# Kernel optimization log

Hardware: AMD Instinct MI355X
Metric: run time of the kernel (lower is better)

Reference implementation:

```python
import jax, jax.numpy as jnp
import numpy as np

B, S, DIN, DIM, H = 2, 2304, 1024, 1024, 16
HEAD_DIM = DIM // H            # 64
ROT_DIM = HEAD_DIM             # partial_rotary_factor = 1
BASE = 10000.0
EPS = 1e-6


def setup_inputs() -> dict:
    key = jax.random.key(0)
    ks = jax.random.split(key, 6)
    return {
        "input": jax.random.normal(ks[0], (B, S, DIN), dtype=jnp.float32),
        "qkv_w": jax.random.normal(ks[1], (3 * DIM, DIN), dtype=jnp.float32) * 0.02,
        "qkv_b": jnp.zeros((3 * DIM,), dtype=jnp.float32),
        "q_scale": jnp.ones((DIM,), dtype=jnp.float32),
        "k_scale": jnp.ones((DIM,), dtype=jnp.float32),
        "proj_w": jax.random.normal(ks[2], (DIN, DIM), dtype=jnp.float32) * 0.02,
        "proj_b": jnp.zeros((DIN,), dtype=jnp.float32),
        "height": 48,
        "width": 48,
    }


def _rms_norm(x, scale):
    # RMSNorm over the full inner dim (QKNorm), learned scale
    var = jnp.mean(x * x, axis=-1, keepdims=True)
    return x * jax.lax.rsqrt(var + EPS) * scale


def _rope_1d(x, pos):
    # x: (b, n, h, d_ax), pos: (n,) float; rotate_half-style RoPE
    d = x.shape[-1]
    inv_freq = 1.0 / (BASE ** (jnp.arange(0, d, 2, dtype=jnp.float32) / d))  # (d/2,)
    ang = pos[:, None] * inv_freq                                            # (n, d/2)
    cos = jnp.concatenate([jnp.cos(ang), jnp.cos(ang)], axis=-1)[None, :, None, :]
    sin = jnp.concatenate([jnp.sin(ang), jnp.sin(ang)], axis=-1)[None, :, None, :]
    x1, x2 = jnp.split(x, 2, axis=-1)
    rot = jnp.concatenate([-x2, x1], axis=-1)
    return x * cos + rot * sin


def _rope_2d(x, height, width):
    # axial 2D RoPE: first half of rotary dims keyed by row, second half by col
    n = height * width
    idx = jnp.arange(n, dtype=jnp.float32)
    rows = jnp.floor(idx / width)
    cols = jnp.mod(idx, width)
    half = ROT_DIM // 2
    x_r = _rope_1d(x[..., :half], rows)
    x_c = _rope_1d(x[..., half:ROT_DIM], cols)
    return jnp.concatenate([x_r, x_c, x[..., ROT_DIM:]], axis=-1)


def reference(input, qkv_w, qkv_b, q_scale, k_scale, proj_w, proj_b, height, width):
    b, n, _ = input.shape
    qkv = input @ qkv_w.T + qkv_b                       # (b, n, 3*dim)
    q, k, v = jnp.split(qkv, 3, axis=-1)
    q = _rms_norm(q, q_scale)
    k = _rms_norm(k, k_scale)
    # (b, n, h, d)
    q = q.reshape(b, n, H, HEAD_DIM)
    k = k.reshape(b, n, H, HEAD_DIM)
    v = v.reshape(b, n, H, HEAD_DIM)
    q = _rope_2d(q, height, width)
    k = _rope_2d(k, height, width)
    scale = HEAD_DIM ** (-0.5)
    # (b, h, q, k)
    scores = jnp.einsum("bqhd,bkhd->bhqk", q, k) * scale
    attn = jax.nn.softmax(scores, axis=-1)
    out = jnp.einsum("bhqk,bkhd->bqhd", attn, v)        # (b, n, h, d)
    out = out.reshape(b, n, DIM)
    return out @ proj_w.T + proj_b
```

## Files before the change

kernel.cpp:

```cpp
#include <hip/hip_runtime.h>
#include <math.h>

#define BB   2
#define SS   2304
#define DINC 1024
#define DIMC 1024
#define HH   16
#define HD   64

typedef _Float16 half_t;
typedef __attribute__((ext_vector_type(4))) _Float16 half4;
typedef __attribute__((ext_vector_type(8))) _Float16 half8;
typedef __attribute__((ext_vector_type(4))) float    f32x4;

#define LOG2E 1.44269504088896340736f
#define EXP2(x) __builtin_amdgcn_exp2f(x)

#define GLOAD_LDS16(gp, lp)                                                     \
    __builtin_amdgcn_global_load_lds(                                           \
        (const __attribute__((address_space(1))) void*)(gp),                    \
        (__attribute__((address_space(3))) void*)(lp), 16, 0, 0)

template<int RB>
__global__ __launch_bounds__(256)
void convert_tile_f16(const float* __restrict__ src, half_t* __restrict__ dst, int K)
{
    constexpr int NG = RB * 32 / 1024;
    const int mb = blockIdx.x;
    const int kb = blockIdx.y;
    const int t  = threadIdx.x;
    const float* sp0 = src + (size_t)mb * RB * K + kb * 32;
    half_t*      dp0 = dst + ((size_t)mb * (K >> 5) + kb) * (RB * 32);
    #pragma unroll
    for (int g = 0; g < NG; ++g) {
        const int e  = g * 1024 + t * 4;
        const int mm = e >> 5, kk = e & 31;
        float4 v = *(const float4*)(sp0 + (size_t)mm * K + kk);
        dp0[e + 0] = (half_t)v.x; dp0[e + 1] = (half_t)v.y;
        dp0[e + 2] = (half_t)v.z; dp0[e + 3] = (half_t)v.w;
    }
}

__global__ __launch_bounds__(256, 3)
void gemm_mfma192(const half_t* __restrict__ Ah, const half_t* __restrict__ Bh,
                  const float* __restrict__ bias, half_t* __restrict__ Cout)
{
    const int t    = threadIdx.x;
    const int w    = t >> 6;
    const int lane = t & 63;
    const int l15  = lane & 15, quad = lane >> 4;
    const int wr   = w >> 1;
    const int wc   = w & 1;
    const int mb   = blockIdx.y;
    const int nb   = blockIdx.x;

    __shared__ __align__(16) half_t As[2][6144];
    __shared__ __align__(16) half_t Bs[2][3072];

    f32x4 acc[6][3];
    #pragma unroll
    for (int mt = 0; mt < 6; ++mt)
        #pragma unroll
        for (int nt = 0; nt < 3; ++nt) acc[mt][nt] = (f32x4){0.f, 0.f, 0.f, 0.f};

    const half_t* atile = Ah + (size_t)mb * 32 * 6144;
    const half_t* btile = Bh + (size_t)nb * 32 * 3072;

    for (int kb = 0; kb < 32; kb += 2) {
        #pragma unroll
        for (int u = 0; u < 2; ++u) {
            const half_t* at = atile + (size_t)(kb + u) * 6144;
            const half_t* bt = btile + (size_t)(kb + u) * 3072;
            for (int ch = w; ch < 18; ch += 4) {
                if (ch < 12) GLOAD_LDS16(at + ch * 512 + lane * 8, &As[u][ch * 512]);
                else         GLOAD_LDS16(bt + (ch - 12) * 512 + lane * 8,
                                         &Bs[u][(ch - 12) * 512]);
            }
        }
        __syncthreads();

        #pragma unroll
        for (int u = 0; u < 2; ++u) {
            half8 af[6], bf[3];
            #pragma unroll
            for (int mt = 0; mt < 6; ++mt)
                af[mt] = *(const half8*)(&As[u][(wr * 96 + mt * 16 + l15) * 32 + quad * 8]);
            #pragma unroll
            for (int nt = 0; nt < 3; ++nt)
                bf[nt] = *(const half8*)(&Bs[u][(wc * 48 + nt * 16 + l15) * 32 + quad * 8]);
            #pragma unroll
            for (int mt = 0; mt < 6; ++mt)
                #pragma unroll
                for (int nt = 0; nt < 3; ++nt)
                    acc[mt][nt] = __builtin_amdgcn_mfma_f32_16x16x32_f16(
                        af[mt], bf[nt], acc[mt][nt], 0, 0, 0);
        }
        __syncthreads();
    }

    const int bm = mb * 192, bn = nb * 96;
    #pragma unroll
    for (int nt = 0; nt < 3; ++nt) {
        const int n  = bn + wc * 48 + nt * 16 + l15;
        const float bv = bias[n];
        #pragma unroll
        for (int mt = 0; mt < 6; ++mt) {
            const int m0 = bm + wr * 96 + mt * 16 + quad * 4;
            #pragma unroll
            for (int rg = 0; rg < 4; ++rg)
                Cout[(size_t)(m0 + rg) * 3072 + n] = (half_t)(acc[mt][nt][rg] + bv);
        }
    }
}

template<int BN, bool OUT_HALF>
__global__ __launch_bounds__(256)
void gemm_mfma(const half_t* __restrict__ Ah, const half_t* __restrict__ Bh,
               const float* __restrict__ bias, void* __restrict__ Cout,
               int M, int N, int K)
{
    constexpr int MT = (BN == 128) ? 4 : 2;
    constexpr int NT = 4;
    const int KB = K >> 5;
    __shared__ half_t As[8192];
    __shared__ half_t Bs[2 * BN * 32];

    const int t    = threadIdx.x;
    const int w    = t >> 6;
    const int lane = t & 63;
    const int l15  = lane & 15, quad = lane >> 4;
    const int wr   = (BN == 128) ? (w >> 1) : w;
    const int wc   = (BN == 128) ? (w & 1) : 0;
    const int mb   = blockIdx.y, nb = blockIdx.x;

    f32x4 acc[MT][NT];
    #pragma unroll
    for (int mt = 0; mt < MT; ++mt)
        #pragma unroll
        for (int nt = 0; nt < NT; ++nt) acc[mt][nt] = (f32x4){0.f, 0.f, 0.f, 0.f};

    const half_t* atile = Ah + (size_t)mb * KB * 4096;
    const half_t* btile = Bh + (size_t)nb * KB * (BN * 32);

    for (int kb = 0; kb < KB; kb += 2) {
        #pragma unroll
        for (int u = 0; u < 2; ++u) {
            const half_t* at = atile + (size_t)(kb + u) * 4096;
            const half_t* bt = btile + (size_t)(kb + u) * (BN * 32);
            #pragma unroll
            for (int v = 0; v < 2; ++v) {
                const int ch = w * 2 + v;
                GLOAD_LDS16(at + ch * 512 + lane * 8, As + u * 4096 + ch * 512);
            }
            GLOAD_LDS16(bt + w * 512 + lane * 8, Bs + u * (BN * 32) + w * 512);
        }
        __syncthreads();

        #pragma unroll
        for (int u = 0; u < 2; ++u) {
            half8 af[MT], bf[NT];
            #pragma unroll
            for (int mt = 0; mt < MT; ++mt)
                af[mt] = *(const half8*)(As + u * 4096
                                         + (wr * (MT * 16) + mt * 16 + l15) * 32 + quad * 8);
            #pragma unroll
            for (int nt = 0; nt < NT; ++nt)
                bf[nt] = *(const half8*)(Bs + u * (BN * 32)
                                         + (wc * 64 + nt * 16 + l15) * 32 + quad * 8);
            #pragma unroll
            for (int mt = 0; mt < MT; ++mt)
                #pragma unroll
                for (int nt = 0; nt < NT; ++nt)
                    acc[mt][nt] = __builtin_amdgcn_mfma_f32_16x16x32_f16(
                        af[mt], bf[nt], acc[mt][nt], 0, 0, 0);
        }
        __syncthreads();
    }

    const int bm = mb * 128, bn = nb * BN;
    #pragma unroll
    for (int nt = 0; nt < NT; ++nt) {
        const int n  = bn + wc * 64 + nt * 16 + l15;
        const float bv = bias[n];
        #pragma unroll
        for (int mt = 0; mt < MT; ++mt) {
            const int m0 = bm + wr * (MT * 16) + mt * 16 + quad * 4;
            #pragma unroll
            for (int rg = 0; rg < 4; ++rg) {
                const float v = acc[mt][nt][rg] + bv;
                if (OUT_HALF) ((half_t*)Cout)[(size_t)(m0 + rg) * N + n] = (half_t)v;
                else          ((float*) Cout)[(size_t)(m0 + rg) * N + n] = v;
            }
        }
    }
}

__global__ __launch_bounds__(256)
void normrope_v7(half_t* __restrict__ qkvh, const float* __restrict__ q_scale,
                 const float* __restrict__ k_scale, const int* __restrict__ wptr,
                 half_t* __restrict__ Kf, half_t* __restrict__ Vf)
{
    const int token = blockIdx.x;
    const int s     = token % SS;
    const int b     = token / SS;
    const int w     = *wptr;
    const int t     = threadIdx.x;
    const float rowp = (float)(s / w);
    const float colp = (float)(s % w);

    half_t* base = qkvh + (size_t)token * 3072;

    const int c    = s >> 5;
    const int slot = s & 31;
    const int ktile = (slot >> 2) & 1;
    const int krow  = ((slot >> 3) << 2) + (slot & 3);

    {
        half4 v4 = *(const half4*)(base + 2048 + 4 * t);
        const int dabs0 = 4 * t;
        const int h  = dabs0 >> 6;
        const int sl3 = slot >> 3, sl7 = slot & 7;
        half_t* vdst = Vf + ((size_t)(b * HH + h) * 72 + c) * 2048;
        #pragma unroll
        for (int ii = 0; ii < 4; ++ii) {
            const int d = (dabs0 + ii) & 63;
            vdst[(d >> 4) * 512 + (sl3 * 16 + (d & 15)) * 8 + sl7] = v4[ii];
        }
    }

    __shared__ float buf[DIMC];
    __shared__ float red[4];

    #pragma unroll
    for (int sel = 0; sel < 2; ++sel) {
        half_t* row = base + sel * DIMC;
        const float* scp = sel ? k_scale : q_scale;

        half4 xh = *(const half4*)(row + 4 * t);
        float x0 = (float)xh[0], x1 = (float)xh[1], x2 = (float)xh[2], x3 = (float)xh[3];
        float ss = x0 * x0 + x1 * x1 + x2 * x2 + x3 * x3;
        #pragma unroll
        for (int o = 32; o >= 1; o >>= 1) ss += __shfl_xor(ss, o);
        if ((t & 63) == 0) red[t >> 6] = ss;
        __syncthreads();

        const float rinv = rsqrtf((red[0] + red[1] + red[2] + red[3]) * (1.0f / DIMC) + 1e-6f);
        float4 g = *(const float4*)(scp + 4 * t);
        buf[4 * t + 0] = x0 * rinv * g.x;
        buf[4 * t + 1] = x1 * rinv * g.y;
        buf[4 * t + 2] = x2 * rinv * g.z;
        buf[4 * t + 3] = x3 * rinv * g.w;
        __syncthreads();

        const float qsc = sel ? 1.0f : (0.125f * LOG2E);

        #pragma unroll
        for (int pp = 0; pp < 2; ++pp) {
            const int p = t + pp * 256;
            const int h = p >> 5;
            const int r = p & 31;
            const int j = r & 15;
            const float pos = (r < 16) ? rowp : colp;
            const int d1 = (r < 16) ? j : (32 + j);
            const int d2 = d1 + 16;
            const float freq = exp2f((float)j * -0.83048202372f);
            const float ang  = pos * freq;
            float sn, cs;
            __sincosf(ang, &sn, &cs);
            const float a1 = buf[h * HD + d1], a2 = buf[h * HD + d2];
            const float o1 = (a1 * cs - a2 * sn) * qsc;
            const float o2 = (a2 * cs + a1 * sn) * qsc;
            if (sel == 0) {
                row[h * HD + d1] = (half_t)o1;
                row[h * HD + d2] = (half_t)o2;
            } else {
                half_t* kdst = Kf + ((size_t)(b * HH + h) * 72 + c) * 2048;
                kdst[((ktile << 1) + (d1 >> 5)) * 512
                     + ((((d1 & 31) >> 3) << 4) + krow) * 8 + (d1 & 7)] = (half_t)o1;
                kdst[((ktile << 1) + (d2 >> 5)) * 512
                     + ((((d2 & 31) >> 3) << 4) + krow) * 8 + (d2 & 7)] = (half_t)o2;
            }
        }
        __syncthreads();
    }
}

__global__ __launch_bounds__(256, 3)
void flash_attn_mfma17(const half_t* __restrict__ qkvh, const half_t* __restrict__ Kf,
                       const half_t* __restrict__ Vf, half_t* __restrict__ attn_h)
{
    const int flat = blockIdx.x;
    const int xcd  = flat & 7;
    const int idx  = flat >> 3;
    const int bh   = xcd * 4 + idx / 24;
    const int qtb  = idx % 24;
    const int b    = bh >> 4, h = bh & 15;
    const int t    = threadIdx.x;
    const int w    = t >> 6;
    const int qh   = w >> 1;
    const int jt   = w & 1;
    const int lane = t & 63;
    const int l15  = lane & 15, quad = lane >> 4;

    const size_t tb = (size_t)b * SS;
    const int q0 = qtb * 96;

    __shared__ float mlb[4][48];
    __shared__ float Ob[2][64][49];

    half8 qf[3][2];
    #pragma unroll
    for (int qt = 0; qt < 3; ++qt)
        #pragma unroll
        for (int dg = 0; dg < 2; ++dg)
            qf[qt][dg] = *(const half8*)(qkvh + (tb + q0 + qh * 48 + qt * 16 + l15) * 3072
                                          + h * HD + dg * 32 + quad * 8);

    const half8 onesA = (l15 == 0)
        ? (half8){(half_t)1, (half_t)1, (half_t)1, (half_t)1,
                  (half_t)1, (half_t)1, (half_t)1, (half_t)1}
        : (half8){(half_t)0, (half_t)0, (half_t)0, (half_t)0,
                  (half_t)0, (half_t)0, (half_t)0, (half_t)0};

    f32x4 acc[4][3];
    f32x4 acc5[3];
    #pragma unroll
    for (int qt = 0; qt < 3; ++qt) {
        acc5[qt] = (f32x4){0.f, 0.f, 0.f, 0.f};
        #pragma unroll
        for (int dt = 0; dt < 4; ++dt) acc[dt][qt] = (f32x4){0.f, 0.f, 0.f, 0.f};
    }

    const half_t* kpl = Kf + (size_t)bh * 147456 + jt * 2048 + lane * 8;
    const half_t* vpl = Vf + (size_t)bh * 147456 + jt * 2048 + lane * 8;

    half8 k00 = *(const half8*)(kpl);
    half8 k01 = *(const half8*)(kpl + 512);
    half8 k10 = *(const half8*)(kpl + 1024);
    half8 k11 = *(const half8*)(kpl + 1536);
    half8 v0  = *(const half8*)(vpl);
    half8 v1  = *(const half8*)(vpl + 512);
    half8 v2  = *(const half8*)(vpl + 1024);
    half8 v3  = *(const half8*)(vpl + 1536);

    const f32x4 initC = (f32x4){-4.f, -4.f, -4.f, -4.f};

    for (int p = 0; p < 36; ++p) {
        f32x4 scA[3], scB[3];
        __builtin_amdgcn_s_setprio(1);
        #pragma unroll
        for (int qt = 0; qt < 3; ++qt) {
            scA[qt] = initC;
            scA[qt] = __builtin_amdgcn_mfma_f32_16x16x32_f16(k00, qf[qt][0], scA[qt], 0, 0, 0);
            scA[qt] = __builtin_amdgcn_mfma_f32_16x16x32_f16(k01, qf[qt][1], scA[qt], 0, 0, 0);
            scB[qt] = initC;
            scB[qt] = __builtin_amdgcn_mfma_f32_16x16x32_f16(k10, qf[qt][0], scB[qt], 0, 0, 0);
            scB[qt] = __builtin_amdgcn_mfma_f32_16x16x32_f16(k11, qf[qt][1], scB[qt], 0, 0, 0);
        }
        __builtin_amdgcn_s_setprio(0);

        if (p + 1 < 36) {
            const half_t* kN = kpl + (size_t)(p + 1) * 4096;
            k00 = *(const half8*)(kN);
            k01 = *(const half8*)(kN + 512);
            k10 = *(const half8*)(kN + 1024);
            k11 = *(const half8*)(kN + 1536);
        }

        half8 pf[3];
        #pragma unroll
        for (int qt = 0; qt < 3; ++qt) {
            const float a0 = EXP2(scA[qt][0]);
            const float a1 = EXP2(scA[qt][1]);
            const float a2 = EXP2(scA[qt][2]);
            const float a3 = EXP2(scA[qt][3]);
            const float b0 = EXP2(scB[qt][0]);
            const float b1 = EXP2(scB[qt][1]);
            const float b2 = EXP2(scB[qt][2]);
            const float b3 = EXP2(scB[qt][3]);
            pf[qt] = (half8){(half_t)a0, (half_t)a1, (half_t)a2, (half_t)a3,
                             (half_t)b0, (half_t)b1, (half_t)b2, (half_t)b3};
        }

        __builtin_amdgcn_s_setprio(1);
        #pragma unroll
        for (int dt = 0; dt < 4; ++dt) {
            const half8 vf = (dt == 0) ? v0 : (dt == 1) ? v1 : (dt == 2) ? v2 : v3;
            #pragma unroll
            for (int qt = 0; qt < 3; ++qt)
                acc[dt][qt] = __builtin_amdgcn_mfma_f32_16x16x32_f16(
                    vf, pf[qt], acc[dt][qt], 0, 0, 0);
        }
        #pragma unroll
        for (int qt = 0; qt < 3; ++qt)
            acc5[qt] = __builtin_amdgcn_mfma_f32_16x16x32_f16(
                onesA, pf[qt], acc5[qt], 0, 0, 0);
        __builtin_amdgcn_s_setprio(0);

        if (p + 1 < 36) {
            const half_t* vN = vpl + (size_t)(p + 1) * 4096;
            v0 = *(const half8*)(vN);
            v1 = *(const half8*)(vN + 512);
            v2 = *(const half8*)(vN + 1024);
            v3 = *(const half8*)(vN + 1536);
        }
    }

    #pragma unroll
    for (int qt = 0; qt < 3; ++qt)
        if (quad == 0) mlb[w][qt * 16 + l15] = acc5[qt][0];
    __syncthreads();

    float fac[3];
    #pragma unroll
    for (int qt = 0; qt < 3; ++qt) {
        const int q = qt * 16 + l15;
        fac[qt] = 1.0f / (mlb[qh * 2 + 0][q] + mlb[qh * 2 + 1][q]);
    }

    #pragma unroll
    for (int ph = 0; ph < 2; ++ph) {
        if (jt == ph) {
            #pragma unroll
            for (int dt = 0; dt < 4; ++dt)
                #pragma unroll
                for (int qt = 0; qt < 3; ++qt)
                    #pragma unroll
                    for (int rg = 0; rg < 4; ++rg) {
                        const int d = dt * 16 + quad * 4 + rg;
                        const int q = qt * 16 + l15;
                        const float v = acc[dt][qt][rg] * fac[qt];
                        if (ph == 0) Ob[qh][d][q] = v;
                        else         Ob[qh][d][q] += v;
                    }
        }
        __syncthreads();
    }

    #pragma unroll
    for (int g2 = 0; g2 < 3; ++g2) {
        const int q  = g2 * 32 + (t >> 3);
        const int ds = (t & 7) * 8;
        const int qh2 = (q >= 48) ? 1 : 0;
        const int qq  = q - 48 * qh2;
        const size_t mrow = tb + q0 + q;
        const int mb2 = (int)(mrow >> 7);
        const int mm  = (int)(mrow & 127);
        const int kb2 = (h * HD + ds) >> 5;
        const int kk  = ds & 31;
        half8 o;
        #pragma unroll
        for (int ii = 0; ii < 8; ++ii) o[ii] = (half_t)Ob[qh2][ds + ii][qq];
        *(half8*)(attn_h + ((size_t)mb2 * 32 + kb2) * 4096 + mm * 32 + kk) = o;
    }
}

extern "C" void kernel_launch(void* const* d_in, const int* in_sizes, int n_in,
                              void* d_out, int out_size, void* d_ws, size_t ws_size,
                              hipStream_t stream)
{
    const float* input   = (const float*)d_in[0];
    const float* qkv_w   = (const float*)d_in[1];
    const float* qkv_b   = (const float*)d_in[2];
    const float* q_scale = (const float*)d_in[3];
    const float* k_scale = (const float*)d_in[4];
    const float* proj_w  = (const float*)d_in[5];
    const float* proj_b  = (const float*)d_in[6];
    const int*   width   = (const int*)d_in[8];
    float* out = (float*)d_out;

    half_t* qkvh   = (half_t*)d_ws;
    half_t* attn_h = qkvh   + (size_t)4608 * 3072;
    half_t* Vf     = attn_h + (size_t)4608 * 1024;
    half_t* Ah     = Vf     + (size_t)32 * 72 * 2048;
    half_t* Bh1    = Ah     + (size_t)4608 * 1024;
    half_t* Bh2    = Bh1    + (size_t)3072 * 1024;
    half_t* Kf     = Ah;

    const int M = BB * SS;

    convert_tile_f16<192><<<dim3(M / 192, DINC / 32),        256, 0, stream>>>(input,  Ah,  DINC);
    convert_tile_f16<96><<<dim3(3 * DIMC / 96, DINC / 32),   256, 0, stream>>>(qkv_w, Bh1, DINC);
    convert_tile_f16<64><<<dim3(DINC / 64, DIMC / 32),       256, 0, stream>>>(proj_w, Bh2, DIMC);

    gemm_mfma192<<<dim3(3 * DIMC / 96, M / 192), 256, 0, stream>>>(
        Ah, Bh1, qkv_b, qkvh);

    normrope_v7<<<M, 256, 0, stream>>>(qkvh, q_scale, k_scale, width, Kf, Vf);

    flash_attn_mfma17<<<dim3(768), 256, 0, stream>>>(qkvh, Kf, Vf, attn_h);

    gemm_mfma<64, false><<<dim3(DINC / 64, M / 128), 256, 0, stream>>>(
        attn_h, Bh2, proj_b, out, M, DINC, DIMC);
}
```

Before: 228.0 us.

## Retile output projection GEMM to 96x64 blocks matching attention tile layout

Replaces the generic 128-row output projection GEMM with a dedicated 96x64 tile kernel whose 2x2 waves each compute 48x32. The attention kernel now writes its fp16 output straight into the 96-row tiled layout that kernel reads. The grid grows from 576 to 768 blocks, and the launch bound of 3 blocks per SM is meant to improve occupancy and load balance across the GPU's compute units. In exchange, each block reuses its A and B tiles less than before.

```diff
diff --git a/kernel.cpp b/kernel.cpp
--- a/kernel.cpp
+++ b/kernel.cpp
@@ -113,84 +113,74 @@
     }
 }
 
-template<int BN, bool OUT_HALF>
-__global__ __launch_bounds__(256)
-void gemm_mfma(const half_t* __restrict__ Ah, const half_t* __restrict__ Bh,
-               const float* __restrict__ bias, void* __restrict__ Cout,
-               int M, int N, int K)
-{
-    constexpr int MT = (BN == 128) ? 4 : 2;
-    constexpr int NT = 4;
-    const int KB = K >> 5;
-    __shared__ half_t As[8192];
-    __shared__ half_t Bs[2 * BN * 32];
-
+__global__ __launch_bounds__(256, 3)
+void gemm2_mfma96(const half_t* __restrict__ Ah, const half_t* __restrict__ Bh,
+                  const float* __restrict__ bias, float* __restrict__ Cout)
+{
     const int t    = threadIdx.x;
     const int w    = t >> 6;
     const int lane = t & 63;
     const int l15  = lane & 15, quad = lane >> 4;
-    const int wr   = (BN == 128) ? (w >> 1) : w;
-    const int wc   = (BN == 128) ? (w & 1) : 0;
-    const int mb   = blockIdx.y, nb = blockIdx.x;
-
-    f32x4 acc[MT][NT];
-    #pragma unroll
-    for (int mt = 0; mt < MT; ++mt)
-        #pragma unroll
-        for (int nt = 0; nt < NT; ++nt) acc[mt][nt] = (f32x4){0.f, 0.f, 0.f, 0.f};
-
-    const half_t* atile = Ah + (size_t)mb * KB * 4096;
-    const half_t* btile = Bh + (size_t)nb * KB * (BN * 32);
-
-    for (int kb = 0; kb < KB; kb += 2) {
+    const int wr   = w >> 1;
+    const int wc   = w & 1;
+    const int nb   = blockIdx.x;
+    const int mb   = blockIdx.y;
+
+    __shared__ __align__(16) half_t As[2][3072];
+    __shared__ __align__(16) half_t Bs[2][2048];
+
+    f32x4 acc[3][2];
+    #pragma unroll
+    for (int mt = 0; mt < 3; ++mt)
+        #pragma unroll
+        for (int nt = 0; nt < 2; ++nt) acc[mt][nt] = (f32x4){0.f, 0.f, 0.f, 0.f};
+
+    const half_t* atile = Ah + (size_t)mb * 32 * 3072;
+    const half_t* btile = Bh + (size_t)nb * 32 * 2048;
+
+    for (int kb = 0; kb < 32; kb += 2) {
         #pragma unroll
         for (int u = 0; u < 2; ++u) {
-            const half_t* at = atile + (size_t)(kb + u) * 4096;
-            const half_t* bt = btile + (size_t)(kb + u) * (BN * 32);
-            #pragma unroll
-            for (int v = 0; v < 2; ++v) {
-                const int ch = w * 2 + v;
-                GLOAD_LDS16(at + ch * 512 + lane * 8, As + u * 4096 + ch * 512);
+            const half_t* at = atile + (size_t)(kb + u) * 3072;
+            const half_t* bt = btile + (size_t)(kb + u) * 2048;
+            for (int ch = w; ch < 10; ch += 4) {
+                if (ch < 6) GLOAD_LDS16(at + ch * 512 + lane * 8, &As[u][ch * 512]);
+                else        GLOAD_LDS16(bt + (ch - 6) * 512 + lane * 8,
+                                        &Bs[u][(ch - 6) * 512]);
             }
-            GLOAD_LDS16(bt + w * 512 + lane * 8, Bs + u * (BN * 32) + w * 512);
         }
         __syncthreads();
 
         #pragma unroll
         for (int u = 0; u < 2; ++u) {
-            half8 af[MT], bf[NT];
-            #pragma unroll
-            for (int mt = 0; mt < MT; ++mt)
-                af[mt] = *(const half8*)(As + u * 4096
-                                         + (wr * (MT * 16) + mt * 16 + l15) * 32 + quad * 8);
-            #pragma unroll
-            for (int nt = 0; nt < NT; ++nt)
-                bf[nt] = *(const half8*)(Bs + u * (BN * 32)
-                                         + (wc * 64 + nt * 16 + l15) * 32 + quad * 8);
-            #pragma unroll
-            for (int mt = 0; mt < MT; ++mt)
+            half8 af[3], bf[2];
+            #pragma unroll
+            for (int mt = 0; mt < 3; ++mt)
+                af[mt] = *(const half8*)(&As[u][(wr * 48 + mt * 16 + l15) * 32 + quad * 8]);
+            #pragma unroll
+            for (int nt = 0; nt < 2; ++nt)
+                bf[nt] = *(const half8*)(&Bs[u][(wc * 32 + nt * 16 + l15) * 32 + quad * 8]);
+            #pragma unroll
+            for (int mt = 0; mt < 3; ++mt)
                 #pragma unroll
-                for (int nt = 0; nt < NT; ++nt)
+                for (int nt = 0; nt < 2; ++nt)
                     acc[mt][nt] = __builtin_amdgcn_mfma_f32_16x16x32_f16(
                         af[mt], bf[nt], acc[mt][nt], 0, 0, 0);
         }
         __syncthreads();
     }
 
-    const int bm = mb * 128, bn = nb * BN;
-    #pragma unroll
-    for (int nt = 0; nt < NT; ++nt) {
-        const int n  = bn + wc * 64 + nt * 16 + l15;
+    const int bm = mb * 96, bn = nb * 64;
+    #pragma unroll
+    for (int nt = 0; nt < 2; ++nt) {
+        const int n  = bn + wc * 32 + nt * 16 + l15;
         const float bv = bias[n];
         #pragma unroll
-        for (int mt = 0; mt < MT; ++mt) {
-            const int m0 = bm + wr * (MT * 16) + mt * 16 + quad * 4;
-            #pragma unroll
-            for (int rg = 0; rg < 4; ++rg) {
-                const float v = acc[mt][nt][rg] + bv;
-                if (OUT_HALF) ((half_t*)Cout)[(size_t)(m0 + rg) * N + n] = (half_t)v;
-                else          ((float*) Cout)[(size_t)(m0 + rg) * N + n] = v;
-            }
+        for (int mt = 0; mt < 3; ++mt) {
+            const int m0 = bm + wr * 48 + mt * 16 + quad * 4;
+            #pragma unroll
+            for (int rg = 0; rg < 4; ++rg)
+                Cout[(size_t)(m0 + rg) * 1024 + n] = acc[mt][nt][rg] + bv;
         }
     }
 }
@@ -437,21 +427,21 @@
         __syncthreads();
     }
 
-    #pragma unroll
-    for (int g2 = 0; g2 < 3; ++g2) {
-        const int q  = g2 * 32 + (t >> 3);
-        const int ds = (t & 7) * 8;
-        const int qh2 = (q >= 48) ? 1 : 0;
-        const int qq  = q - 48 * qh2;
-        const size_t mrow = tb + q0 + q;
-        const int mb2 = (int)(mrow >> 7);
-        const int mm  = (int)(mrow & 127);
-        const int kb2 = (h * HD + ds) >> 5;
-        const int kk  = ds & 31;
-        half8 o;
-        #pragma unroll
-        for (int ii = 0; ii < 8; ++ii) o[ii] = (half_t)Ob[qh2][ds + ii][qq];
-        *(half8*)(attn_h + ((size_t)mb2 * 32 + kb2) * 4096 + mm * 32 + kk) = o;
+    {
+        const int ab32 = (int)((tb + q0) / 96) * 32;
+        #pragma unroll
+        for (int g2 = 0; g2 < 3; ++g2) {
+            const int q  = g2 * 32 + (t >> 3);
+            const int ds = (t & 7) * 8;
+            const int qh2 = (q >= 48) ? 1 : 0;
+            const int qq  = q - 48 * qh2;
+            const int kb2 = (h * HD + ds) >> 5;
+            const int kk  = ds & 31;
+            half8 o;
+            #pragma unroll
+            for (int ii = 0; ii < 8; ++ii) o[ii] = (half_t)Ob[qh2][ds + ii][qq];
+            *(half8*)(attn_h + (size_t)(ab32 + kb2) * 3072 + q * 32 + kk) = o;
+        }
     }
 }
 
@@ -490,6 +480,6 @@
 
     flash_attn_mfma17<<<dim3(768), 256, 0, stream>>>(qkvh, Kf, Vf, attn_h);
 
-    gemm_mfma<64, false><<<dim3(DINC / 64, M / 128), 256, 0, stream>>>(
-        attn_h, Bh2, proj_b, out, M, DINC, DIMC);
-}
+    gemm2_mfma96<<<dim3(DINC / 64, M / 96), 256, 0, stream>>>(
+        attn_h, Bh2, proj_b, out);
+}
```

Result: slower. 238.7 us (+4.7%).
